# Kernel tuning notes

Hardware: AMD Instinct MI355X
Metric: run time of the kernel (lower is better)

## Reference

```python
import jax, jax.numpy as jnp
import numpy as np

# ---- circuit constants (from init_kwargs) ----
KERNEL = 4
STRIDE = 2
PAD = 0
W_Q = 4            # data wires (AmplitudeEmbedding of 16 values)
D_Q = 2            # discarded wires (swap-test reference, start in |0>)
N_Q = W_Q + D_Q + 1  # + ancilla; ancilla is wire N_Q-1 (last tensor axis)
MPS_LAYERS = 2
N_BLOCKS = W_Q // 1 - 1  # qml.MPS: n_wires//(n_block_wires//2) - 1 = 3
N_PARAMS_BLOCK = 2

_SQ2 = 1.0 / np.sqrt(2.0)
H_GATE = np.array([[_SQ2, _SQ2], [_SQ2, -_SQ2]], dtype=np.float32)
CNOT = np.array([[1, 0, 0, 0], [0, 1, 0, 0], [0, 0, 0, 1], [0, 0, 1, 0]], dtype=np.float32)
_csw = np.eye(8, dtype=np.float32)
_csw[5, 5] = 0.0; _csw[6, 6] = 0.0; _csw[5, 6] = 1.0; _csw[6, 5] = 1.0  # |1ab> -> |1ba>
CSWAP = _csw


def apply_gate(state, U, wires):
    # state: (2,)*N_Q tensor; U: (2^k, 2^k); wires: tuple of k axes
    k = len(wires)
    U = U.reshape((2,) * (2 * k))
    state = jnp.tensordot(U, state, axes=(tuple(range(k, 2 * k)), wires))
    return jnp.moveaxis(state, tuple(range(k)), wires)


def ry(theta):
    c, s = jnp.cos(theta / 2.0), jnp.sin(theta / 2.0)
    return jnp.stack([jnp.stack([c, -s]), jnp.stack([s, c])])


def circuit(patch, weights_mps):
    # patch: (16,) real amplitudes; whole circuit is real -> real statevector is exact
    norm = jnp.linalg.norm(patch)
    e0 = jnp.zeros(2 ** W_Q, patch.dtype).at[0].set(1.0)
    amp = jnp.where(norm > 0, patch / jnp.maximum(norm, 1e-12), e0)
    # wires 0..D-1 in |0>, wires D..D+W-1 hold amp, ancilla |0>
    state = jnp.zeros((2 ** D_Q, 2 ** W_Q, 2), patch.dtype).at[0, :, 0].set(amp)
    state = state.reshape((2,) * N_Q)
    anc = N_Q - 1
    state = apply_gate(state, jnp.asarray(H_GATE), (anc,))
    for l in range(MPS_LAYERS):
        for b in range(N_BLOCKS):
            w0, w1 = D_Q + b, D_Q + b + 1
            state = apply_gate(state, ry(weights_mps[l, b, 0]), (w0,))
            state = apply_gate(state, ry(weights_mps[l, b, 1]), (w1,))
            state = apply_gate(state, jnp.asarray(CNOT), (w0, w1))
    for i in range(D_Q):
        state = apply_gate(state, jnp.asarray(CSWAP), (anc, i, i + D_Q))
    state = apply_gate(state, jnp.asarray(H_GATE), (anc,))
    # probs of PauliZ on ancilla, take P(0); ancilla is the last axis
    return jnp.sum(state[..., 0] ** 2)


def setup_inputs() -> dict:
    key = jax.random.key(0)
    k1, k2 = jax.random.split(key)
    img = jax.random.uniform(k1, (256, 1, 64, 64), dtype=jnp.float32)
    weights_mps = jax.random.normal(k2, (MPS_LAYERS, N_BLOCKS, N_PARAMS_BLOCK), dtype=jnp.float32)
    return {"img": img, "weights_mps": weights_mps}


def reference(img, weights_mps):
    bs = img.shape[0]
    if PAD > 0:
        img = jnp.pad(img, ((0, 0), (0, 0), (PAD, PAD), (PAD, PAD)))
    # vectorized im2col; feature order (kh, kw) matches the original nested loop
    pat = jax.lax.conv_general_dilated_patches(
        img[:, :1], filter_shape=(KERNEL, KERNEL), window_strides=(STRIDE, STRIDE), padding='VALID')
    oh, ow = pat.shape[2], pat.shape[3]
    pat = jnp.moveaxis(pat, 1, -1).reshape(-1, KERNEL * KERNEL)  # (bs*oh*ow, 16)
    p0 = jax.vmap(lambda p: circuit(p, weights_mps))(pat)
    return p0.reshape(bs, 1, oh * ow)
```

## Files before the change

kernel.cpp:

```cpp
#include <hip/hip_runtime.h>
#include <math.h>

#define BS     256
#define IMG_H  64
#define IMG_W  64
#define OH     31
#define OW     31
#define NPOS   (OH * OW)
#define NPATCH (BS * NPOS)

__device__ __forceinline__ void ry_on(float* st, int bit, float c, float s) {
    const int m = 1 << bit;
#pragma unroll
    for (int i = 0; i < 16; ++i) {
        if (!(i & m)) {
            float a0 = st[i];
            float a1 = st[i | m];
            st[i]     = c * a0 - s * a1;
            st[i | m] = s * a0 + c * a1;
        }
    }
}

__device__ __forceinline__ void cnot_on(float* st, int cb, int tb) {
    const int cm = 1 << cb, tm = 1 << tb;
#pragma unroll
    for (int i = 0; i < 16; ++i) {
        if ((i & cm) && !(i & tm)) {
            float tmp = st[i];
            st[i] = st[i | tm];
            st[i | tm] = tmp;
        }
    }
}

__global__ __launch_bounds__(256) void encoder_kernel(
    const float* __restrict__ img,
    const float* __restrict__ wmps,
    float* __restrict__ out)
{
    __shared__ float sc[12], ss[12];
    const int t = threadIdx.x;
    if (t < 12) {
        float th = 0.5f * wmps[t];
        sc[t] = cosf(th);
        ss[t] = sinf(th);
    }
    __syncthreads();

    const int idx = blockIdx.x * 256 + t;
    const int b   = idx / NPOS;
    const int pos = idx - b * NPOS;
    const int oi  = pos / OW;
    const int oj  = pos - oi * OW;

    const float2* base2 = (const float2*)(img + ((size_t)b * IMG_H + (size_t)(oi * 2)) * IMG_W)
                          + oj;

    float st[16];
    float n2 = 0.0f;
#pragma unroll
    for (int kh = 0; kh < 4; ++kh) {
        float2 lo = base2[kh * (IMG_W / 2)];
        float2 hi = base2[kh * (IMG_W / 2) + 1];
        st[kh * 4 + 0] = lo.x;
        st[kh * 4 + 1] = lo.y;
        st[kh * 4 + 2] = hi.x;
        st[kh * 4 + 3] = hi.y;
        n2 += lo.x * lo.x + lo.y * lo.y + hi.x * hi.x + hi.y * hi.y;
    }

    if (n2 <= 0.0f) { st[0] = 1.0f; n2 = 1.0f; }

#pragma unroll
    for (int l = 0; l < 2; ++l) {
#pragma unroll
        for (int blk = 0; blk < 3; ++blk) {
            const int wi = (l * 3 + blk) * 2;
            ry_on(st, 3 - blk, sc[wi],     ss[wi]);
            ry_on(st, 2 - blk, sc[wi + 1], ss[wi + 1]);
            cnot_on(st, 3 - blk, 2 - blk);
        }
    }

    float num = st[0] * st[0] + st[1] * st[1] + st[2] * st[2] + st[3] * st[3];
    out[idx] = 0.5f * (1.0f + num * __builtin_amdgcn_rcpf(n2));
}

extern "C" void kernel_launch(void* const* d_in, const int* in_sizes, int n_in,
                              void* d_out, int out_size, void* d_ws, size_t ws_size,
                              hipStream_t stream) {
    const float* img  = (const float*)d_in[0];
    const float* wmps = (const float*)d_in[1];
    float* out = (float*)d_out;

    encoder_kernel<<<NPATCH / 256, 256, 0, stream>>>(img, wmps, out);
}
```

Measured before the change: 9.827 us.

## Precompute fused MPS unitary rows in a tiny kernel and apply as matvec

A separate single-block kernel applies the whole RY/CNOT sequence to each basis vector once, producing the 4 needed rows of the composed 16x16 unitary in workspace. The main kernel then replaces the per-patch gate simulation with a 4x16 matrix-vector product using uniform loads of M, and drops the shared-memory trig and barrier. This cuts per-thread arithmetic but adds a second kernel launch and a global-memory dependency between kernels.

```diff
diff --git a/kernel.cpp b/kernel.cpp
--- a/kernel.cpp
+++ b/kernel.cpp
@@ -34,21 +34,47 @@
     }
 }
 
+__global__ __launch_bounds__(64) void build_m_kernel(
+    const float* __restrict__ wmps,
+    float* __restrict__ M)
+{
+    const int t = threadIdx.x;
+    if (t >= 16) return;
+
+    float c[12], s[12];
+#pragma unroll
+    for (int i = 0; i < 12; ++i) {
+        float th = 0.5f * wmps[i];
+        c[i] = cosf(th);
+        s[i] = sinf(th);
+    }
+
+    float st[16];
+#pragma unroll
+    for (int i = 0; i < 16; ++i) st[i] = 0.0f;
+    st[t] = 1.0f;
+
+#pragma unroll
+    for (int l = 0; l < 2; ++l) {
+#pragma unroll
+        for (int blk = 0; blk < 3; ++blk) {
+            const int wi = (l * 3 + blk) * 2;
+            ry_on(st, 3 - blk, c[wi],     s[wi]);
+            ry_on(st, 2 - blk, c[wi + 1], s[wi + 1]);
+            cnot_on(st, 3 - blk, 2 - blk);
+        }
+    }
+
+#pragma unroll
+    for (int j = 0; j < 4; ++j) M[j * 16 + t] = st[j];
+}
+
 __global__ __launch_bounds__(256) void encoder_kernel(
     const float* __restrict__ img,
-    const float* __restrict__ wmps,
+    const float* __restrict__ M,
     float* __restrict__ out)
 {
-    __shared__ float sc[12], ss[12];
-    const int t = threadIdx.x;
-    if (t < 12) {
-        float th = 0.5f * wmps[t];
-        sc[t] = cosf(th);
-        ss[t] = sinf(th);
-    }
-    __syncthreads();
-
-    const int idx = blockIdx.x * 256 + t;
+    const int idx = blockIdx.x * 256 + threadIdx.x;
     const int b   = idx / NPOS;
     const int pos = idx - b * NPOS;
     const int oi  = pos / OW;
@@ -57,33 +83,32 @@
     const float2* base2 = (const float2*)(img + ((size_t)b * IMG_H + (size_t)(oi * 2)) * IMG_W)
                           + oj;
 
-    float st[16];
+    float p[16];
     float n2 = 0.0f;
 #pragma unroll
     for (int kh = 0; kh < 4; ++kh) {
         float2 lo = base2[kh * (IMG_W / 2)];
         float2 hi = base2[kh * (IMG_W / 2) + 1];
-        st[kh * 4 + 0] = lo.x;
-        st[kh * 4 + 1] = lo.y;
-        st[kh * 4 + 2] = hi.x;
-        st[kh * 4 + 3] = hi.y;
+        p[kh * 4 + 0] = lo.x;
+        p[kh * 4 + 1] = lo.y;
+        p[kh * 4 + 2] = hi.x;
+        p[kh * 4 + 3] = hi.y;
         n2 += lo.x * lo.x + lo.y * lo.y + hi.x * hi.x + hi.y * hi.y;
     }
 
-    if (n2 <= 0.0f) { st[0] = 1.0f; n2 = 1.0f; }
+    if (n2 <= 0.0f) { p[0] = 1.0f; n2 = 1.0f; }
 
+    float a0 = 0.0f, a1 = 0.0f, a2 = 0.0f, a3 = 0.0f;
 #pragma unroll
-    for (int l = 0; l < 2; ++l) {
-#pragma unroll
-        for (int blk = 0; blk < 3; ++blk) {
-            const int wi = (l * 3 + blk) * 2;
-            ry_on(st, 3 - blk, sc[wi],     ss[wi]);
-            ry_on(st, 2 - blk, sc[wi + 1], ss[wi + 1]);
-            cnot_on(st, 3 - blk, 2 - blk);
-        }
+    for (int t = 0; t < 16; ++t) {
+        const float pv = p[t];
+        a0 = fmaf(M[t],      pv, a0);
+        a1 = fmaf(M[16 + t], pv, a1);
+        a2 = fmaf(M[32 + t], pv, a2);
+        a3 = fmaf(M[48 + t], pv, a3);
     }
 
-    float num = st[0] * st[0] + st[1] * st[1] + st[2] * st[2] + st[3] * st[3];
+    const float num = a0 * a0 + a1 * a1 + a2 * a2 + a3 * a3;
     out[idx] = 0.5f * (1.0f + num * __builtin_amdgcn_rcpf(n2));
 }
 
@@ -93,6 +118,8 @@
     const float* img  = (const float*)d_in[0];
     const float* wmps = (const float*)d_in[1];
     float* out = (float*)d_out;
+    float* M   = (float*)d_ws;
 
-    encoder_kernel<<<NPATCH / 256, 256, 0, stream>>>(img, wmps, out);
+    build_m_kernel<<<1, 64, 0, stream>>>(wmps, M);
+    encoder_kernel<<<NPATCH / 256, 256, 0, stream>>>(img, M, out);
 }
```

New measurement: 12.09 us. +23.0%, slower.

## Precompute circuit unitary rows per block and apply as 4x16 matvec

Applied to the files above, without the earlier changes.

The first 16 threads of each block push basis vectors through the gate sequence to build the four needed rows of the linear map in shared memory. Each thread then computes those four outputs as a 4x16 dot product instead of applying every RY and CNOT gate. The global loads are issued before the barrier so their latency overlaps the matrix setup. In exchange, every block now pays for a small serial setup phase and a second barrier, and each thread reads 64 floats from shared memory.

```diff
diff --git a/kernel.cpp b/kernel.cpp
--- a/kernel.cpp
+++ b/kernel.cpp
@@ -40,13 +40,34 @@
     float* __restrict__ out)
 {
     __shared__ float sc[12], ss[12];
+    __shared__ float sM[64];
     const int t = threadIdx.x;
+
     if (t < 12) {
         float th = 0.5f * wmps[t];
         sc[t] = cosf(th);
         ss[t] = sinf(th);
     }
     __syncthreads();
+
+    if (t < 16) {
+        float st[16];
+#pragma unroll
+        for (int i = 0; i < 16; ++i) st[i] = 0.0f;
+        st[t] = 1.0f;
+#pragma unroll
+        for (int l = 0; l < 2; ++l) {
+#pragma unroll
+            for (int blk = 0; blk < 3; ++blk) {
+                const int wi = (l * 3 + blk) * 2;
+                ry_on(st, 3 - blk, sc[wi],     ss[wi]);
+                ry_on(st, 2 - blk, sc[wi + 1], ss[wi + 1]);
+                cnot_on(st, 3 - blk, 2 - blk);
+            }
+        }
+#pragma unroll
+        for (int j = 0; j < 4; ++j) sM[j * 16 + t] = st[j];
+    }
 
     const int idx = blockIdx.x * 256 + t;
     const int b   = idx / NPOS;
@@ -57,33 +78,45 @@
     const float2* base2 = (const float2*)(img + ((size_t)b * IMG_H + (size_t)(oi * 2)) * IMG_W)
                           + oj;
 
-    float st[16];
+    float2 r[8];
+#pragma unroll
+    for (int kh = 0; kh < 4; ++kh) {
+        r[kh * 2]     = base2[kh * (IMG_W / 2)];
+        r[kh * 2 + 1] = base2[kh * (IMG_W / 2) + 1];
+    }
+
+    __syncthreads();
+
+    float p[16];
     float n2 = 0.0f;
 #pragma unroll
-    for (int kh = 0; kh < 4; ++kh) {
-        float2 lo = base2[kh * (IMG_W / 2)];
-        float2 hi = base2[kh * (IMG_W / 2) + 1];
-        st[kh * 4 + 0] = lo.x;
-        st[kh * 4 + 1] = lo.y;
-        st[kh * 4 + 2] = hi.x;
-        st[kh * 4 + 3] = hi.y;
-        n2 += lo.x * lo.x + lo.y * lo.y + hi.x * hi.x + hi.y * hi.y;
+    for (int i = 0; i < 8; ++i) {
+        p[i * 2]     = r[i].x;
+        p[i * 2 + 1] = r[i].y;
+        n2 += r[i].x * r[i].x + r[i].y * r[i].y;
     }
 
-    if (n2 <= 0.0f) { st[0] = 1.0f; n2 = 1.0f; }
+    if (n2 <= 0.0f) { p[0] = 1.0f; n2 = 1.0f; }
 
+    const float4* M4 = (const float4*)sM;
+    const float4* p4 = (const float4*)p;
+    float acc[4];
 #pragma unroll
-    for (int l = 0; l < 2; ++l) {
+    for (int j = 0; j < 4; ++j) {
+        float a = 0.0f;
 #pragma unroll
-        for (int blk = 0; blk < 3; ++blk) {
-            const int wi = (l * 3 + blk) * 2;
-            ry_on(st, 3 - blk, sc[wi],     ss[wi]);
-            ry_on(st, 2 - blk, sc[wi + 1], ss[wi + 1]);
-            cnot_on(st, 3 - blk, 2 - blk);
+        for (int q = 0; q < 4; ++q) {
+            float4 m = M4[j * 4 + q];
+            float4 v = p4[q];
+            a = fmaf(m.x, v.x, a);
+            a = fmaf(m.y, v.y, a);
+            a = fmaf(m.z, v.z, a);
+            a = fmaf(m.w, v.w, a);
         }
+        acc[j] = a;
     }
 
-    float num = st[0] * st[0] + st[1] * st[1] + st[2] * st[2] + st[3] * st[3];
+    const float num = acc[0] * acc[0] + acc[1] * acc[1] + acc[2] * acc[2] + acc[3] * acc[3];
     out[idx] = 0.5f * (1.0f + num * __builtin_amdgcn_rcpf(n2));
 }
 
```

After: 9.738 us. About the same (-0.9%).
